# Optimization experiments

Measured on AMD Instinct MI355X. Metric: run time of the kernel, lower is better.

Reference implementation:

```python
import jax, jax.numpy as jnp
import numpy as np

K = 11  # masked conv3d kernel size

def mask_A(k):
    # mask type 'A': flattened (i,j,t) positions with current_id < k^3//2 + 1
    # (current_id starts at 1) -> first k^3//2 positions are 1.
    m = (np.arange(k ** 3) < (k ** 3) // 2).astype(np.float32).reshape(k, k, k)
    return jnp.asarray(m)

def conv3d(x, w, b, pad):
    out = jax.lax.conv_general_dilated(
        x, w, window_strides=(1, 1, 1), padding=[(pad, pad)] * 3,
        dimension_numbers=('NCDHW', 'OIDHW', 'NCDHW'))
    return out + b[None, :, None, None, None]

def conv2d(x, w, b, pad):
    out = jax.lax.conv_general_dilated(
        x, w, window_strides=(1, 1), padding=[(pad, pad)] * 2,
        dimension_numbers=('NCHW', 'OIHW', 'NCHW'))
    return out + b[None, :, None, None]

def pconv(x, w, b):
    # 1x1x1 conv3d as channel GEMM; w: [O, C]
    return jnp.einsum('bcdhw,oc->bodhw', x, w) + b[None, :, None, None, None]

def _phi(z):
    return 0.5 * (1.0 + jax.lax.erf(z / jnp.sqrt(2.0).astype(z.dtype)))

def setup_inputs() -> dict:
    key = jax.random.key(0)
    ks = jax.random.split(key, 12)
    M = 192
    B, H, W = 1, 48, 48
    s = 0.02
    x = jax.random.normal(ks[0], (B, M, H, W), jnp.float32)
    hyper = jax.random.normal(ks[1], (B, 2 * M, H, W), jnp.float32)
    W3 = s * jax.random.normal(ks[2], (M, 2 * M, 3, 3), jnp.float32)
    b3 = jnp.zeros((M,), jnp.float32)
    W1 = s * jax.random.normal(ks[3], (24, 1, K, K, K), jnp.float32)
    b1 = jnp.zeros((24,), jnp.float32)
    Wa = s * jax.random.normal(ks[4], (48, 25), jnp.float32)
    ba = jnp.zeros((48,), jnp.float32)
    Wb = s * jax.random.normal(ks[5], (96, 48), jnp.float32)
    bb = jnp.zeros((96,), jnp.float32)
    Wc = s * jax.random.normal(ks[6], (9, 96), jnp.float32)
    bc = jnp.zeros((9,), jnp.float32)
    return {"x": x, "hyper": hyper, "W3": W3, "b3": b3, "W1": W1, "b1": b1,
            "Wa": Wa, "ba": ba, "Wb": Wb, "bb": bb, "Wc": Wc, "bc": bc}

def reference(x, hyper, W3, b3, W1, b1, Wa, ba, Wb, bb, Wc, bc):
    # x: [B,M,H,W], hyper: [B,2M,H,W]
    x5 = x[:, None]                                   # [B,1,M,H,W]
    h = conv2d(hyper, W3, b3, 1)[:, None]             # [B,1,M,H,W]
    W1m = W1 * mask_A(K)[None, None]                  # causal mask re-applied each fwd
    x1 = conv3d(x5, W1m, b1, 5)                       # [B,24,M,H,W]
    t = jnp.concatenate([x1, h], axis=1)              # [B,25,M,H,W]
    t = jax.nn.relu(pconv(t, Wa, ba))                 # [B,48,M,H,W]
    t = jax.nn.relu(pconv(t, Wb, bb))                 # [B,96,M,H,W]
    out = pconv(t, Wc, bc)                            # [B,9,M,H,W]
    # 3-component weighted Gaussian entropy model
    mu = out[:, 0:3]
    sc = out[:, 3:6]
    sc = jnp.abs(jnp.where(sc == 0.0, 1e-9, sc))
    w = jax.nn.softmax(out[:, 6:9], axis=1)
    xe = x[:, None]                                   # [B,1,M,H,W]
    lik = jnp.abs(_phi((xe + 0.5 - mu) / sc) - _phi((xe - 0.5 - mu) / sc))
    p3 = jnp.sum(w * lik, axis=1)                     # [B,M,H,W]
    return (p3, out)
```

## Files before the change

### kernel.cpp

```cpp
#include <hip/hip_runtime.h>
#include <hip/hip_fp16.h>
#include <math.h>

#define HW    2304
#define NPOS  442368

typedef _Float16 f16x8 __attribute__((ext_vector_type(8)));
typedef __fp16   h16x2 __attribute__((ext_vector_type(2)));
typedef float    f32x4 __attribute__((ext_vector_type(4)));

__device__ __forceinline__ float phi_f(float z) {
    return 0.5f * (1.0f + erff(z * 0.70710678118654752f));
}
__device__ __forceinline__ unsigned short f2h(float v) {
    _Float16 h = (_Float16)v;
    return *reinterpret_cast<unsigned short*>(&h);
}
__device__ __forceinline__ unsigned int pk2(float a, float b) {
    return (unsigned int)f2h(a) | ((unsigned int)f2h(b) << 16);
}
__device__ __forceinline__ unsigned int pkrtz(float a, float b) {
    h16x2 h = __builtin_amdgcn_cvt_pkrtz(a, b);
    return *reinterpret_cast<unsigned int*>(&h);
}
__device__ __forceinline__ unsigned int bperm(int idx4, unsigned int v) {
    return (unsigned int)__builtin_amdgcn_ds_bpermute(idx4, (int)v);
}

__global__ __launch_bounds__(256) void prep_all(const float* __restrict__ hyper,
                                                const float* __restrict__ W3,
                                                const float* __restrict__ W1,
                                                const float* __restrict__ Wa,
                                                const float* __restrict__ ba,
                                                const float* __restrict__ b1,
                                                const float* __restrict__ Wb,
                                                const float* __restrict__ bb,
                                                const float* __restrict__ Wc,
                                                const float* __restrict__ xg,
                                                unsigned short* __restrict__ hyperTp,
                                                unsigned short* __restrict__ apack,
                                                unsigned short* __restrict__ pk,
                                                unsigned short* __restrict__ xhp) {
    const int bx = blockIdx.x;
    if (bx < 948) {
        __shared__ float s[32][33];
        const int pt = bx % 79, it = bx / 79;
        const int tid = threadIdx.x;
        const int c = tid & 31, r = tid >> 5;
        const int pp = pt * 32 + c;
        const int yp = pp / 50, xp = pp % 50;
        const bool inter = (pp < 2500) && yp >= 1 && yp <= 48 && xp >= 1 && xp <= 48;
        const int src = inter ? ((yp - 1) * 48 + (xp - 1)) : 0;
#pragma unroll
        for (int i = 0; i < 4; ++i) {
            int icl = r + i * 8;
            s[icl][c] = inter ? hyper[(size_t)(it * 32 + icl) * HW + src] : 0.f;
        }
        __syncthreads();
#pragma unroll
        for (int i = 0; i < 4; ++i) {
            int pl = r + i * 8;
            int pp2 = pt * 32 + pl;
            if (pp2 < 2500)
                hyperTp[(size_t)pp2 * 384 + it * 32 + c] = f2h(s[c][pl]);
        }
    } else if (bx < 3540) {
        int idx = (bx - 948) * 256 + threadIdx.x;
        int j = idx & 7;
        int l = (idx >> 3) & 63;
        int rest = idx >> 9;
        int t = rest % 9; rest /= 9;
        int c = rest % 12; int T = rest / 12;
        int oc = T * 16 + (l & 15);
        int ic = c * 32 + (l >> 4) * 8 + j;
        apack[idx] = f2h(W3[((size_t)oc * 384 + ic) * 9 + t]);
    } else if (bx < 3700) {
        int idx = (bx - 3540) * 256 + threadIdx.x;
        if (idx >= 40960) return;
        float v = 0.f;
        if (idx < 31744) {
            int j = idx & 7, lane = (idx >> 3) & 63, s = (idx >> 9) & 1, c = idx >> 10;
            int q = lane >> 4;
            int oc = s * 16 + (lane & 15);
            int r = 2 * c + (q >> 1), h = q & 1, kw = 8 * h + j;
            if (oc < 24 && r < 61 && kw < 11) {
                int kd = r / 11, kh = r % 11;
                int tap = kd * 121 + kh * 11 + kw;
                if (tap < 665) v = W1[oc * 1331 + tap];
            }
        } else if (idx < 33280) {
            int i2 = idx - 31744;
            int j = i2 & 7, lane = (i2 >> 3) & 63, t = i2 >> 9;
            int m = t * 16 + (lane & 15), k = (lane >> 4) * 8 + j;
            if (k < 25) v = Wa[m * 25 + k];
            else if (k == 25) {
                float s = ba[m];
                for (int c = 0; c < 24; ++c) s += Wa[m * 25 + c] * b1[c];
                v = s;
            }
        } else if (idx < 39424) {
            int i3 = idx - 33280;
            int j = i3 & 7, lane = (i3 >> 3) & 63, k2 = (i3 >> 9) & 1, s = i3 >> 10;
            int m = s * 16 + (lane & 15), ch = k2 * 32 + (lane >> 4) * 8 + j;
            if (ch < 48) v = Wb[m * 48 + ch];
            else if (ch == 48) v = bb[m];
        } else {
            int i4 = idx - 39424;
            int j = i4 & 7, lane = (i4 >> 3) & 63, k3 = i4 >> 9;
            int m = lane & 15, ch = k3 * 32 + (lane >> 4) * 8 + j;
            if (m < 9) v = Wc[m * 96 + ch];
        }
        pk[idx] = f2h(v);
    } else {
        int idx = (bx - 3700) * 256 + threadIdx.x;
        if (idx >= 187456) return;
        int si = idx * 4;
        int zp = si / 3712, rem = si - zp * 3712;
        int yp = rem >> 6, xp0 = rem & 63;
        float f[4];
#pragma unroll
        for (int k = 0; k < 4; ++k) {
            int xp = xp0 + k;
            bool in = zp >= 5 && zp < 197 && yp >= 5 && yp < 53 && xp >= 5 && xp < 53;
            f[k] = in ? xg[(size_t)(zp - 5) * HW + (yp - 5) * 48 + (xp - 5)] : 0.f;
        }
        *(uint2*)&xhp[si] = make_uint2(pk2(f[0], f[1]), pk2(f[2], f[3]));
    }
}

__global__ __launch_bounds__(256, 4) void fused3(const unsigned short* __restrict__ xhp,
                                                 const unsigned short* __restrict__ pk,
                                                 const unsigned short* __restrict__ hyperTp,
                                                 const unsigned short* __restrict__ apack,
                                                 const float* __restrict__ b3,
                                                 const float* __restrict__ xg,
                                                 const float* __restrict__ bc,
                                                 float* __restrict__ out) {
    __shared__ __align__(16) unsigned short P[6656];
    __shared__ __align__(16) float hpart[1024];
    __shared__ __align__(16) float htile[256];

    const int tid = threadIdx.x, w = tid >> 6, lane = tid & 63;
    const int n = lane & 15, q = lane >> 4;
    const int bx = blockIdx.x;
    const int x0 = (bx % 12) * 4, y0 = ((bx / 12) % 12) * 4;
    const int T = bx / 144, d0 = T * 16;

#pragma unroll
    for (int k = 0; k < 3; ++k) {
        int idx = tid + k * 256;
        if (idx < 588) {
            int row = idx >> 1, half = idx & 1;
            int py = row / 21, pz = row - py * 21;
            int sw = (row >> 2) & 1;
            const uint4* src = (const uint4*)(xhp + ((size_t)(d0 + pz) * 58 + (y0 + py)) * 64
                                              + x0 + half * 8);
            *(uint4*)&P[row * 16 + ((half ^ sw) << 3)] = *src;
        }
    }

    {
        const int pp = (y0 + (n >> 2)) * 50 + x0 + (n & 3);
        const size_t bbase = (size_t)pp * 384 + q * 8;
        f32x4 hc[3];
#pragma unroll
        for (int cc = 0; cc < 3; ++cc) {
            const int c = w * 3 + cc;
            const unsigned short* ap = apack + ((size_t)(T * 12 + c) * 9) * 512 + lane * 8;
            const int coff = c * 32;
            f32x4 a0 = {0.f, 0.f, 0.f, 0.f};
#pragma unroll
            for (int t = 0; t < 9; ++t) {
                f16x8 a = *(const f16x8*)(ap + t * 512);
                const int dd = (t / 3) * 50 + (t % 3);
                f16x8 b = *(const f16x8*)(hyperTp + bbase + (size_t)dd * 384 + coff);
                a0 = __builtin_amdgcn_mfma_f32_16x16x32_f16(a, b, a0, 0, 0, 0);
            }
            hc[cc] = a0;
        }
#pragma unroll
        for (int e = 0; e < 4; ++e)
            hpart[w * 256 + (q * 4 + e) * 16 + n] = hc[0][e] + hc[1][e] + hc[2][e];
    }
    __syncthreads();

    {
        const int oc = tid >> 4, pos = tid & 15;
        float h = b3[d0 + oc];
#pragma unroll
        for (int ww = 0; ww < 4; ++ww) h += hpart[ww * 256 + oc * 16 + pos];
        htile[oc * 16 + pos] = h;
    }

    const f32x4 zf = {0.f, 0.f, 0.f, 0.f};
    f32x4 acc[4][2];
#pragma unroll
    for (int p = 0; p < 4; ++p) { acc[p][0] = zf; acc[p][1] = zf; }

    const f16x8* Av = (const f16x8*)pk;
    const int hb = q & 1, par = q >> 1;
    const int w21n = w * 21 + n;
#pragma unroll
    for (int c = 0; c < 31; ++c) {
        const int r0 = 2 * c, r1 = 2 * c + 1;
        const int K0 = (r0 % 11) * 21 + (r0 / 11);
        const int K1 = (r1 % 11) * 21 + (r1 / 11);
        const int rowc = w21n + (par ? K1 : K0);
        const int sw = (rowc >> 2) & 1;
        const unsigned short* rp128 = P + rowc * 16 + ((hb ^ sw) << 3);
        const unsigned short* rp64  = P + rowc * 16 + ((1  ^ sw) << 3);
        unsigned int u[6];
        *(uint4*)&u[0] = *(const uint4*)rp128;
        *(uint2*)&u[4] = *(const uint2*)rp64;
        f16x8 ca0 = Av[c * 128 + lane];
        f16x8 ca1 = Av[c * 128 + 64 + lane];
#pragma unroll
        for (int px = 0; px < 4; ++px) {
            unsigned int bw[4];
#pragma unroll
            for (int i = 0; i < 4; ++i) {
                if ((px & 1) == 0) bw[i] = u[(px >> 1) + i];
                else bw[i] = (u[(px >> 1) + i] >> 16) | (u[(px >> 1) + 1 + i] << 16);
            }
            f16x8 bf = *(f16x8*)bw;
            acc[px][0] = __builtin_amdgcn_mfma_f32_16x16x32_f16(ca0, bf, acc[px][0], 0, 0, 0);
            acc[px][1] = __builtin_amdgcn_mfma_f32_16x16x32_f16(ca1, bf, acc[px][1], 0, 0, 0);
        }
    }
    __syncthreads();

#pragma unroll
    for (int px = 0; px < 4; ++px) {
        unsigned int lo = pk2(acc[px][0][0], acc[px][0][1]);
        unsigned int hi = pk2(acc[px][0][2], acc[px][0][3]);
        *(uint2*)&P[(w * 16 + n) * 104 + px * 24 + q * 4] = make_uint2(lo, hi);
        if (q < 2) {
            unsigned int l2 = pk2(acc[px][1][0], acc[px][1][1]);
            unsigned int h2 = pk2(acc[px][1][2], acc[px][1][3]);
            *(uint2*)&P[(w * 16 + n) * 104 + px * 24 + 16 + q * 4] = make_uint2(l2, h2);
        }
    }

    const f16x8* WaF = (const f16x8*)(pk + 31744);
    const f16x8* WbF = (const f16x8*)(pk + 33280);
    const f16x8* WcF = (const f16x8*)(pk + 39424);
    f16x8 waf[3], wbf[12], wcf[3];
#pragma unroll
    for (int s = 0; s < 3; ++s) waf[s] = WaF[s * 64 + lane];
#pragma unroll
    for (int t = 0; t < 12; ++t) wbf[t] = WbF[t * 64 + lane];
#pragma unroll
    for (int k = 0; k < 3; ++k) wcf[k] = WcF[k * 64 + lane];
    float bcv[4];
#pragma unroll
    for (int e = 0; e < 4; ++e) bcv[e] = (q * 4 + e < 9) ? bc[q * 4 + e] : 0.f;

    const int idxg[2] = { (n + 16 * ((2 * q + 0) & 3)) * 4,
                          (n + 16 * ((2 * q + 1) & 3)) * 4 };
    const bool qlo = (q < 2);

    const f16x8 z8 = {};
    for (int px = 0; px < 4; ++px) {
        f16x8 b0;
        if (q < 3) {
            b0 = *(const f16x8*)&P[(w * 16 + n) * 104 + px * 24 + q * 8];
        } else {
            b0 = z8;
            b0[0] = (_Float16)htile[n * 16 + w * 4 + px];
            b0[1] = (_Float16)1.0f;
        }
        unsigned int pw1[6];
#pragma unroll
        for (int s = 0; s < 3; ++s) {
            f32x4 r1 = __builtin_amdgcn_mfma_f32_16x16x32_f16(waf[s], b0, zf, 0, 0, 0);
            pw1[s * 2 + 0] = pkrtz(fmaxf(r1[0], 0.f), fmaxf(r1[1], 0.f));
            pw1[s * 2 + 1] = pkrtz(fmaxf(r1[2], 0.f), fmaxf(r1[3], 0.f));
        }
        unsigned int bpA[3][2][2];
#pragma unroll
        for (int s = 0; s < 3; ++s)
#pragma unroll
            for (int h = 0; h < 2; ++h) {
                bpA[s][h][0] = bperm(idxg[0], pw1[s * 2 + h]);
                bpA[s][h][1] = bperm(idxg[1], pw1[s * 2 + h]);
            }
        unsigned int bf0w[4], bf1w[4];
#pragma unroll
        for (int ww = 0; ww < 4; ++ww) {
            const int h = ww & 1, g = ww >> 1;
            bf0w[ww] = qlo ? bpA[0][h][g] : bpA[1][h][g];
            unsigned int c1 = (q == 2) ? ((ww == 0) ? 0x00003C00u : 0u) : 0u;
            bf1w[ww] = qlo ? bpA[2][h][g] : c1;
        }
        f16x8 bf0 = *(f16x8*)bf0w, bf1 = *(f16x8*)bf1w;
        unsigned int pw2[12];
#pragma unroll
        for (int s = 0; s < 6; ++s) {
            f32x4 rb = __builtin_amdgcn_mfma_f32_16x16x32_f16(wbf[s * 2 + 0], bf0, zf, 0, 0, 0);
            rb = __builtin_amdgcn_mfma_f32_16x16x32_f16(wbf[s * 2 + 1], bf1, rb, 0, 0, 0);
            pw2[s * 2 + 0] = pkrtz(fmaxf(rb[0], 0.f), fmaxf(rb[1], 0.f));
            pw2[s * 2 + 1] = pkrtz(fmaxf(rb[2], 0.f), fmaxf(rb[3], 0.f));
        }
        f32x4 rc = zf;
#pragma unroll
        for (int k3 = 0; k3 < 3; ++k3) {
            unsigned int wv[4];
#pragma unroll
            for (int ww = 0; ww < 4; ++ww) {
                const int h = ww & 1, g = ww >> 1;
                unsigned int lo_ = bperm(idxg[g], pw2[(2 * k3) * 2 + h]);
                unsigned int hi_ = bperm(idxg[g], pw2[(2 * k3 + 1) * 2 + h]);
                wv[ww] = qlo ? lo_ : hi_;
            }
            f16x8 bfc = *(f16x8*)wv;
            rc = __builtin_amdgcn_mfma_f32_16x16x32_f16(wcf[k3], bfc, rc, 0, 0, 0);
        }
        {
            float* pr = (float*)(P + (w * 16 + n) * 104 + px * 24);
#pragma unroll
            for (int e = 0; e < 4; ++e) {
                const int row = q * 4 + e;
                if (row < 9) pr[row] = rc[e] + bcv[e];
            }
        }
    }

    {
        const float* pr = (const float*)(P + (w * 16 + (lane >> 2)) * 104 + (lane & 3) * 24);
        f32x4 oA = *(const f32x4*)pr;
        f32x4 oB = *(const f32x4*)(pr + 4);
        float o8 = pr[8];
        const int gp = (d0 + (lane >> 2)) * HW + (y0 + w) * 48 + x0 + (lane & 3);
        const float xv = xg[gp];
        float m = fmaxf(oB[2], fmaxf(oB[3], o8));
        float e0 = expf(oB[2] - m), e1 = expf(oB[3] - m), e2 = expf(o8 - m);
        float inv_es = 1.0f / (e0 + e1 + e2);
        float mu0 = oA[0], mu1 = oA[1], mu2 = oA[2];
        float s0 = oA[3], s1 = oB[0], s2 = oB[1];
        float p = 0.f;
#pragma unroll
        for (int jj = 0; jj < 3; ++jj) {
            float mu = (jj == 0) ? mu0 : (jj == 1) ? mu1 : mu2;
            float sc = (jj == 0) ? s0 : (jj == 1) ? s1 : s2;
            sc = (sc == 0.0f) ? 1e-9f : sc;
            sc = fabsf(sc);
            float a = phi_f((xv + 0.5f - mu) / sc);
            float b = phi_f((xv - 0.5f - mu) / sc);
            float lik = fabsf(a - b);
            float wgt = ((jj == 0) ? e0 : (jj == 1) ? e1 : e2) * inv_es;
            p = fmaf(wgt, lik, p);
        }
        out[gp] = p;
        out[NPOS + (size_t)0 * NPOS + gp] = mu0;
        out[NPOS + (size_t)1 * NPOS + gp] = mu1;
        out[NPOS + (size_t)2 * NPOS + gp] = mu2;
        out[NPOS + (size_t)3 * NPOS + gp] = s0;
        out[NPOS + (size_t)4 * NPOS + gp] = s1;
        out[NPOS + (size_t)5 * NPOS + gp] = s2;
        out[NPOS + (size_t)6 * NPOS + gp] = oB[2];
        out[NPOS + (size_t)7 * NPOS + gp] = oB[3];
        out[NPOS + (size_t)8 * NPOS + gp] = o8;
    }
}

extern "C" void kernel_launch(void* const* d_in, const int* in_sizes, int n_in,
                              void* d_out, int out_size, void* d_ws, size_t ws_size,
                              hipStream_t stream) {
    const float* x     = (const float*)d_in[0];
    const float* hyper = (const float*)d_in[1];
    const float* W3    = (const float*)d_in[2];
    const float* b3    = (const float*)d_in[3];
    const float* W1    = (const float*)d_in[4];
    const float* b1    = (const float*)d_in[5];
    const float* Wa    = (const float*)d_in[6];
    const float* ba    = (const float*)d_in[7];
    const float* Wb    = (const float*)d_in[8];
    const float* bb    = (const float*)d_in[9];
    const float* Wc    = (const float*)d_in[10];
    const float* bc    = (const float*)d_in[11];
    float* out = (float*)d_out;

    unsigned short* hyperTp = (unsigned short*)d_ws;
    unsigned short* apack   = hyperTp + 960000;
    unsigned short* pk      = apack + 663552;
    unsigned short* xhp     = pk + 40960;

    prep_all<<<4433, 256, 0, stream>>>(hyper, W3, W1, Wa, ba, b1, Wb, bb, Wc, x,
                                       hyperTp, apack, pk, xhp);
    fused3<<<1728, 256, 0, stream>>>(xhp, pk, hyperTp, apack, b3, x, bc, out);
}
```

Measured before the change: 154.0 us.

## Stage pointwise weights in LDS, drop P swizzle, split prep kernel

The Wa/Wb/Wc MFMA fragments are no longer held in registers. They are loaded into registers early, written to a new shared-memory buffer that also holds hpart, and re-read from LDS for each MFMA. This frees VGPRs in fused3, probably to keep the occupancy of 4 waves set by the launch bounds. The XOR bank swizzle on the P tile is removed, which simplifies addressing but can bring back LDS bank conflicts. The combined prep kernel is split into three launches, which adds launch overhead.

```diff
diff --git a/kernel.cpp b/kernel.cpp
--- a/kernel.cpp
+++ b/kernel.cpp
@@ -27,56 +27,58 @@
     return (unsigned int)__builtin_amdgcn_ds_bpermute(idx4, (int)v);
 }
 
-__global__ __launch_bounds__(256) void prep_all(const float* __restrict__ hyper,
-                                                const float* __restrict__ W3,
-                                                const float* __restrict__ W1,
-                                                const float* __restrict__ Wa,
-                                                const float* __restrict__ ba,
-                                                const float* __restrict__ b1,
-                                                const float* __restrict__ Wb,
-                                                const float* __restrict__ bb,
-                                                const float* __restrict__ Wc,
-                                                const float* __restrict__ xg,
-                                                unsigned short* __restrict__ hyperTp,
-                                                unsigned short* __restrict__ apack,
-                                                unsigned short* __restrict__ pk,
-                                                unsigned short* __restrict__ xhp) {
+__global__ __launch_bounds__(256) void prep_hyperTp(const float* __restrict__ hyper,
+                                                    unsigned short* __restrict__ hyperTp) {
+    __shared__ float s[32][33];
     const int bx = blockIdx.x;
-    if (bx < 948) {
-        __shared__ float s[32][33];
-        const int pt = bx % 79, it = bx / 79;
-        const int tid = threadIdx.x;
-        const int c = tid & 31, r = tid >> 5;
-        const int pp = pt * 32 + c;
-        const int yp = pp / 50, xp = pp % 50;
-        const bool inter = (pp < 2500) && yp >= 1 && yp <= 48 && xp >= 1 && xp <= 48;
-        const int src = inter ? ((yp - 1) * 48 + (xp - 1)) : 0;
-#pragma unroll
-        for (int i = 0; i < 4; ++i) {
-            int icl = r + i * 8;
-            s[icl][c] = inter ? hyper[(size_t)(it * 32 + icl) * HW + src] : 0.f;
-        }
-        __syncthreads();
-#pragma unroll
-        for (int i = 0; i < 4; ++i) {
-            int pl = r + i * 8;
-            int pp2 = pt * 32 + pl;
-            if (pp2 < 2500)
-                hyperTp[(size_t)pp2 * 384 + it * 32 + c] = f2h(s[c][pl]);
-        }
-    } else if (bx < 3540) {
-        int idx = (bx - 948) * 256 + threadIdx.x;
-        int j = idx & 7;
-        int l = (idx >> 3) & 63;
-        int rest = idx >> 9;
-        int t = rest % 9; rest /= 9;
-        int c = rest % 12; int T = rest / 12;
-        int oc = T * 16 + (l & 15);
-        int ic = c * 32 + (l >> 4) * 8 + j;
-        apack[idx] = f2h(W3[((size_t)oc * 384 + ic) * 9 + t]);
-    } else if (bx < 3700) {
-        int idx = (bx - 3540) * 256 + threadIdx.x;
-        if (idx >= 40960) return;
+    const int pt = bx % 79, it = bx / 79;
+    const int tid = threadIdx.x;
+    const int c = tid & 31, r = tid >> 5;
+    const int pp = pt * 32 + c;
+    const int yp = pp / 50, xp = pp % 50;
+    const bool inter = (pp < 2500) && yp >= 1 && yp <= 48 && xp >= 1 && xp <= 48;
+    const int src = inter ? ((yp - 1) * 48 + (xp - 1)) : 0;
+#pragma unroll
+    for (int i = 0; i < 4; ++i) {
+        int icl = r + i * 8;
+        s[icl][c] = inter ? hyper[(size_t)(it * 32 + icl) * HW + src] : 0.f;
+    }
+    __syncthreads();
+#pragma unroll
+    for (int i = 0; i < 4; ++i) {
+        int pl = r + i * 8;
+        int pp2 = pt * 32 + pl;
+        if (pp2 < 2500)
+            hyperTp[(size_t)pp2 * 384 + it * 32 + c] = f2h(s[c][pl]);
+    }
+}
+
+__global__ __launch_bounds__(256) void prep_apack(const float* __restrict__ W3,
+                                                  unsigned short* __restrict__ apack) {
+    int idx = blockIdx.x * 256 + threadIdx.x;
+    int j = idx & 7;
+    int l = (idx >> 3) & 63;
+    int rest = idx >> 9;
+    int t = rest % 9; rest /= 9;
+    int c = rest % 12; int T = rest / 12;
+    int oc = T * 16 + (l & 15);
+    int ic = c * 32 + (l >> 4) * 8 + j;
+    apack[idx] = f2h(W3[((size_t)oc * 384 + ic) * 9 + t]);
+}
+
+__global__ __launch_bounds__(256) void prep_rest(const float* __restrict__ W1,
+                                                 const float* __restrict__ Wa,
+                                                 const float* __restrict__ ba,
+                                                 const float* __restrict__ b1,
+                                                 const float* __restrict__ Wb,
+                                                 const float* __restrict__ bb,
+                                                 const float* __restrict__ Wc,
+                                                 const float* __restrict__ xg,
+                                                 unsigned short* __restrict__ pk,
+                                                 unsigned short* __restrict__ xhp) {
+    const int bx = blockIdx.x;
+    if (bx < 160) {
+        int idx = bx * 256 + threadIdx.x;
         float v = 0.f;
         if (idx < 31744) {
             int j = idx & 7, lane = (idx >> 3) & 63, s = (idx >> 9) & 1, c = idx >> 10;
@@ -112,7 +114,7 @@
         }
         pk[idx] = f2h(v);
     } else {
-        int idx = (bx - 3700) * 256 + threadIdx.x;
+        int idx = (bx - 160) * 256 + threadIdx.x;
         if (idx >= 187456) return;
         int si = idx * 4;
         int zp = si / 3712, rem = si - zp * 3712;
@@ -137,8 +139,8 @@
                                                  const float* __restrict__ bc,
                                                  float* __restrict__ out) {
     __shared__ __align__(16) unsigned short P[6656];
-    __shared__ __align__(16) float hpart[1024];
     __shared__ __align__(16) float htile[256];
+    __shared__ __align__(16) unsigned short WU[9216];
 
     const int tid = threadIdx.x, w = tid >> 6, lane = tid & 63;
     const int n = lane & 15, q = lane >> 4;
@@ -146,16 +148,17 @@
     const int x0 = (bx % 12) * 4, y0 = ((bx / 12) % 12) * 4;
     const int T = bx / 144, d0 = T * 16;
 
+    float* hpart = (float*)WU;
+
 #pragma unroll
     for (int k = 0; k < 3; ++k) {
         int idx = tid + k * 256;
         if (idx < 588) {
             int row = idx >> 1, half = idx & 1;
             int py = row / 21, pz = row - py * 21;
-            int sw = (row >> 2) & 1;
             const uint4* src = (const uint4*)(xhp + ((size_t)(d0 + pz) * 58 + (y0 + py)) * 64
                                               + x0 + half * 8);
-            *(uint4*)&P[row * 16 + ((half ^ sw) << 3)] = *src;
+            *(uint4*)&P[row * 16 + half * 8] = *src;
         }
     }
 
@@ -192,26 +195,29 @@
         htile[oc * 16 + pos] = h;
     }
 
+    const uint4* pkW4 = (const uint4*)(pk + 31744);
+    uint4 wreg[4], wreg4;
+#pragma unroll
+    for (int k = 0; k < 4; ++k) wreg[k] = pkW4[tid + k * 256];
+    wreg4 = (tid < 128) ? pkW4[tid + 1024] : make_uint4(0u, 0u, 0u, 0u);
+
     const f32x4 zf = {0.f, 0.f, 0.f, 0.f};
     f32x4 acc[4][2];
 #pragma unroll
     for (int p = 0; p < 4; ++p) { acc[p][0] = zf; acc[p][1] = zf; }
 
     const f16x8* Av = (const f16x8*)pk;
-    const int hb = q & 1, par = q >> 1;
-    const int w21n = w * 21 + n;
+    const int par = q >> 1;
+    const unsigned short* Pb = P + (w * 21 + n) * 16 + (q & 1) * 8;
 #pragma unroll
     for (int c = 0; c < 31; ++c) {
         const int r0 = 2 * c, r1 = 2 * c + 1;
-        const int K0 = (r0 % 11) * 21 + (r0 / 11);
-        const int K1 = (r1 % 11) * 21 + (r1 / 11);
-        const int rowc = w21n + (par ? K1 : K0);
-        const int sw = (rowc >> 2) & 1;
-        const unsigned short* rp128 = P + rowc * 16 + ((hb ^ sw) << 3);
-        const unsigned short* rp64  = P + rowc * 16 + ((1  ^ sw) << 3);
+        const int o0 = ((r0 % 11) * 21 + (r0 / 11)) * 16;
+        const int o1 = ((r1 % 11) * 21 + (r1 / 11)) * 16;
+        const unsigned short* rp = Pb + (par ? o1 : o0);
         unsigned int u[6];
-        *(uint4*)&u[0] = *(const uint4*)rp128;
-        *(uint2*)&u[4] = *(const uint2*)rp64;
+        *(uint4*)&u[0] = *(const uint4*)rp;
+        *(uint2*)&u[4] = *(const uint2*)(rp + 8);
         f16x8 ca0 = Av[c * 128 + lane];
         f16x8 ca1 = Av[c * 128 + 64 + lane];
 #pragma unroll
@@ -240,17 +246,17 @@
             *(uint2*)&P[(w * 16 + n) * 104 + px * 24 + 16 + q * 4] = make_uint2(l2, h2);
         }
     }
-
-    const f16x8* WaF = (const f16x8*)(pk + 31744);
-    const f16x8* WbF = (const f16x8*)(pk + 33280);
-    const f16x8* WcF = (const f16x8*)(pk + 39424);
-    f16x8 waf[3], wbf[12], wcf[3];
-#pragma unroll
-    for (int s = 0; s < 3; ++s) waf[s] = WaF[s * 64 + lane];
-#pragma unroll
-    for (int t = 0; t < 12; ++t) wbf[t] = WbF[t * 64 + lane];
-#pragma unroll
-    for (int k = 0; k < 3; ++k) wcf[k] = WcF[k * 64 + lane];
+    {
+        uint4* WU4 = (uint4*)WU;
+#pragma unroll
+        for (int k = 0; k < 4; ++k) WU4[tid + k * 256] = wreg[k];
+        if (tid < 128) WU4[tid + 1024] = wreg4;
+    }
+    __syncthreads();
+
+    const unsigned short* WaL = WU;
+    const unsigned short* WbL = WU + 1536;
+    const unsigned short* WcL = WU + 7680;
     float bcv[4];
 #pragma unroll
     for (int e = 0; e < 4; ++e) bcv[e] = (q * 4 + e < 9) ? bc[q * 4 + e] : 0.f;
@@ -272,7 +278,8 @@
         unsigned int pw1[6];
 #pragma unroll
         for (int s = 0; s < 3; ++s) {
-            f32x4 r1 = __builtin_amdgcn_mfma_f32_16x16x32_f16(waf[s], b0, zf, 0, 0, 0);
+            f16x8 a = *(const f16x8*)&WaL[(s * 64 + lane) * 8];
+            f32x4 r1 = __builtin_amdgcn_mfma_f32_16x16x32_f16(a, b0, zf, 0, 0, 0);
             pw1[s * 2 + 0] = pkrtz(fmaxf(r1[0], 0.f), fmaxf(r1[1], 0.f));
             pw1[s * 2 + 1] = pkrtz(fmaxf(r1[2], 0.f), fmaxf(r1[3], 0.f));
         }
@@ -296,8 +303,10 @@
         unsigned int pw2[12];
 #pragma unroll
         for (int s = 0; s < 6; ++s) {
-            f32x4 rb = __builtin_amdgcn_mfma_f32_16x16x32_f16(wbf[s * 2 + 0], bf0, zf, 0, 0, 0);
-            rb = __builtin_amdgcn_mfma_f32_16x16x32_f16(wbf[s * 2 + 1], bf1, rb, 0, 0, 0);
+            f16x8 a0w = *(const f16x8*)&WbL[((s * 2 + 0) * 64 + lane) * 8];
+            f16x8 a1w = *(const f16x8*)&WbL[((s * 2 + 1) * 64 + lane) * 8];
+            f32x4 rb = __builtin_amdgcn_mfma_f32_16x16x32_f16(a0w, bf0, zf, 0, 0, 0);
+            rb = __builtin_amdgcn_mfma_f32_16x16x32_f16(a1w, bf1, rb, 0, 0, 0);
             pw2[s * 2 + 0] = pkrtz(fmaxf(rb[0], 0.f), fmaxf(rb[1], 0.f));
             pw2[s * 2 + 1] = pkrtz(fmaxf(rb[2], 0.f), fmaxf(rb[3], 0.f));
         }
@@ -313,7 +322,8 @@
                 wv[ww] = qlo ? lo_ : hi_;
             }
             f16x8 bfc = *(f16x8*)wv;
-            rc = __builtin_amdgcn_mfma_f32_16x16x32_f16(wcf[k3], bfc, rc, 0, 0, 0);
+            f16x8 aw = *(const f16x8*)&WcL[(k3 * 64 + lane) * 8];
+            rc = __builtin_amdgcn_mfma_f32_16x16x32_f16(aw, bfc, rc, 0, 0, 0);
         }
         {
             float* pr = (float*)(P + (w * 16 + n) * 104 + px * 24);
@@ -385,7 +395,8 @@
     unsigned short* pk      = apack + 663552;
     unsigned short* xhp     = pk + 40960;
 
-    prep_all<<<4433, 256, 0, stream>>>(hyper, W3, W1, Wa, ba, b1, Wb, bb, Wc, x,
-                                       hyperTp, apack, pk, xhp);
+    prep_hyperTp<<<948, 256, 0, stream>>>(hyper, hyperTp);
+    prep_apack<<<2592, 256, 0, stream>>>(W3, apack);
+    prep_rest<<<893, 256, 0, stream>>>(W1, Wa, ba, b1, Wb, bb, Wc, x, pk, xhp);
     fused3<<<1728, 256, 0, stream>>>(xhp, pk, hyperTp, apack, b3, x, bc, out);
 }
```

Result: slower. 160.2 us (+4.1%).
